# Kernel tuning notes

Measured on AMD Instinct MI355X. Metric: run time of the kernel, lower is better.

Reference implementation:

```python
import jax, jax.numpy as jnp
import numpy as np

B, N, D = 4, 2048, 512
H, DA, DL = 8, 64, 64  # heads, attention_dim, linear_dim
EPS = 1e-6


def _layer_norm(x, eps=EPS):
    # F.layer_norm with no affine params
    mu = jnp.mean(x, axis=-1, keepdims=True)
    var = jnp.var(x, axis=-1, keepdims=True)
    return (x - mu) * jax.lax.rsqrt(var + eps)


def setup_inputs() -> dict:
    key = jax.random.key(0)
    k1, k2, k3, k4 = jax.random.split(key, 4)
    x = jax.random.normal(k1, (B, N, D), dtype=jnp.float32)
    # causal (lower-triangular) valid-attention mask, float {0,1}, shape (B,1,N,N)
    attention_mask = jnp.broadcast_to(
        jnp.tril(jnp.ones((N, N), dtype=jnp.float32))[None, None], (B, 1, N, N)
    )
    # _uvqk: (D, 2*H*DL + 2*H*DA), init normal(0, 0.02)
    uvqk = 0.02 * jax.random.normal(k2, (D, 2 * H * DL + 2 * H * DA), dtype=jnp.float32)
    # _o: Linear(H*DL -> D), xavier uniform
    fan_in, fan_out = H * DL, D
    limit = float(np.sqrt(6.0 / (fan_in + fan_out)))
    o_weight = jax.random.uniform(k3, (fan_out, fan_in), dtype=jnp.float32, minval=-limit, maxval=limit)
    o_bias = jnp.zeros((D,), dtype=jnp.float32)
    return {"x": x, "attention_mask": attention_mask, "uvqk": uvqk,
            "o_weight": o_weight, "o_bias": o_bias}


def reference(x, attention_mask, uvqk, o_weight, o_bias):
    b, n, _ = x.shape
    normed_x = _layer_norm(x)
    mm = jax.nn.silu(normed_x @ uvqk)  # fused uvqk projection + silu
    u, v, q, k = jnp.split(mm, [H * DL, 2 * H * DL, 2 * H * DL + H * DA], axis=-1)
    qh = q.reshape(b, n, H, DA)
    kh = k.reshape(b, n, H, DA)
    vh = v.reshape(b, n, H, DL)
    # silu-activated (non-softmax) attention with mask
    qk = jnp.einsum('bnhd,bmhd->bhnm', qh, kh)
    qk = jax.nn.silu(qk) / n
    qk = qk * attention_mask  # (B,1,N,N) broadcast over heads
    attn = jnp.einsum('bhnm,bmhd->bnhd', qk, vh).reshape(b, n, H * DL)
    # gated norm + output proj + residual
    o_input = u * _layer_norm(attn)
    return o_input @ o_weight.T + o_bias + x
```

## Files before the change

### kernel.cpp

```cpp
#include <hip/hip_runtime.h>

typedef __bf16 bf16x8 __attribute__((ext_vector_type(8)));
typedef float f32x4 __attribute__((ext_vector_type(4)));
typedef float f32x16 __attribute__((ext_vector_type(16)));
typedef int i32x2 __attribute__((ext_vector_type(2)));

__device__ __forceinline__ unsigned short f2bf(float f) {
  return __builtin_bit_cast(unsigned short, (__bf16)f);
}
__device__ __forceinline__ float bfu2f(unsigned short b) {
  unsigned int u = ((unsigned int)b) << 16;
  return __builtin_bit_cast(float, u);
}
__device__ __forceinline__ float silu_f(float x) {
  return x * __builtin_amdgcn_rcpf(1.0f + __expf(-x));
}
__device__ __forceinline__ unsigned pk2(float a, float b) {
  return (unsigned)f2bf(a) | ((unsigned)f2bf(b) << 16);
}

template<int CPR, int NI, int SWZ>
__device__ __forceinline__ void stage16(const __bf16* __restrict__ g, int ld,
                                        __bf16* lds, int wave, int lane) {
#pragma unroll
  for (int t = 0; t < NI; ++t) {
    int cb = (wave * NI + t) * 64;
    int c = cb + lane;
    int row = c / CPR;
    int colb = (c % CPR) ^ (row & SWZ);
    __builtin_amdgcn_global_load_lds(
        (const __attribute__((address_space(1))) unsigned int*)(g + row * ld + colb * 8),
        (__attribute__((address_space(3))) unsigned int*)(lds + cb * 8),
        16, 0, 0);
  }
}

__global__ void k_prep(const float* __restrict__ x, __bf16* __restrict__ nx,
                       const float* __restrict__ ow, __bf16* __restrict__ owb,
                       const float* __restrict__ uvqk, __bf16* __restrict__ uvqkT) {
  int bid = blockIdx.x, tid = threadIdx.x;
  if (bid < 4096) {
    int t = tid & 127;
    int r = bid * 2 + (tid >> 7);
    int wave = tid >> 6;
    float4 v = ((const float4*)(x + (size_t)r * 512))[t];
    float s = v.x + v.y + v.z + v.w;
    float ss = v.x * v.x + v.y * v.y + v.z * v.z + v.w * v.w;
#pragma unroll
    for (int o = 32; o > 0; o >>= 1) { s += __shfl_down(s, o); ss += __shfl_down(ss, o); }
    __shared__ float red[4][2];
    if ((tid & 63) == 0) { red[wave][0] = s; red[wave][1] = ss; }
    __syncthreads();
    int rw = (wave >> 1) * 2;
    s = red[rw][0] + red[rw + 1][0];
    ss = red[rw][1] + red[rw + 1][1];
    float mu = s * (1.0f / 512.0f);
    float var = ss * (1.0f / 512.0f) - mu * mu;
    float rs = rsqrtf(var + 1e-6f);
    ushort4 o4;
    o4.x = f2bf((v.x - mu) * rs); o4.y = f2bf((v.y - mu) * rs);
    o4.z = f2bf((v.z - mu) * rs); o4.w = f2bf((v.w - mu) * rs);
    ((ushort4*)(nx + (size_t)r * 512))[t] = o4;
  } else if (bid < 4352) {
    int i = (bid - 4096) * 256 + tid;
    float4 v = ((const float4*)ow)[i];
    ushort4 o4;
    o4.x = f2bf(v.x); o4.y = f2bf(v.y); o4.z = f2bf(v.z); o4.w = f2bf(v.w);
    ((ushort4*)owb)[i] = o4;
  } else {
    __shared__ float tile[32][33];
    int bb = bid - 4352;
    int n0 = (bb & 63) * 32, k0 = (bb >> 6) * 32;
    int tx = tid & 31, ty = tid >> 5;
    for (int i = ty; i < 32; i += 8)
      tile[i][tx] = uvqk[(k0 + i) * 2048 + n0 + tx];
    __syncthreads();
    for (int i = ty; i < 32; i += 8)
      uvqkT[(n0 + i) * 512 + k0 + tx] = (__bf16)tile[tx][i];
  }
}

__global__ __launch_bounds__(256, 2) void k_proj(
    const __bf16* __restrict__ A, const __bf16* __restrict__ Bt,
    __bf16* __restrict__ u, __bf16* __restrict__ qn,
    __bf16* __restrict__ kn, __bf16* __restrict__ vt) {
  __shared__ __bf16 As[128 * 64];
  __shared__ __bf16 Bs[256 * 64];
  int tid = threadIdx.x, wave = tid >> 6, lane = tid & 63;
  int lr = lane & 15, lq = lane >> 4;
  int bn = blockIdx.x, bm = blockIdx.y;
  const __bf16* Ag = A + (size_t)bm * 128 * 512;
  const __bf16* Bg = Bt + (size_t)bn * 256 * 512;
  int wm = (wave >> 1) * 64, wn2 = (wave & 1) * 128;
  f32x4 acc[4][8] = {};
  for (int k0 = 0; k0 < 512; k0 += 64) {
    stage16<8, 4, 7>(Ag + k0, 512, As, wave, lane);
    stage16<8, 8, 7>(Bg + k0, 512, Bs, wave, lane);
    __syncthreads();
#pragma unroll
    for (int kk = 0; kk < 2; ++kk) {
      int b = kk * 4 + lq;
      bf16x8 a[4], bb[8];
#pragma unroll
      for (int i = 0; i < 4; ++i) {
        int row = wm + i * 16 + lr;
        a[i] = *(const bf16x8*)(As + row * 64 + ((b ^ (row & 7)) * 8));
      }
#pragma unroll
      for (int j = 0; j < 8; ++j) {
        int row = wn2 + j * 16 + lr;
        bb[j] = *(const bf16x8*)(Bs + row * 64 + ((b ^ (row & 7)) * 8));
      }
#pragma unroll
      for (int i = 0; i < 4; ++i)
#pragma unroll
        for (int j = 0; j < 8; ++j)
          acc[i][j] = __builtin_amdgcn_mfma_f32_16x16x32_bf16(a[i], bb[j], acc[i][j], 0, 0, 0);
    }
    __syncthreads();
  }
  int seg = bn >> 1;
  int cb = (bn & 1) * 256 + wn2;
  int rb0 = bm * 128 + wm + lq * 4;
  if (seg == 1) {
#pragma unroll
    for (int i = 0; i < 4; ++i) {
      int rb = rb0 + i * 16;
      int b = rb >> 11, n = rb & 2047;
#pragma unroll
      for (int j = 0; j < 8; ++j) {
        int c = cb + j * 16 + lr;
        ushort4 w;
        w.x = f2bf(silu_f(acc[i][j][0]) * (1.0f / 2048.0f));
        w.y = f2bf(silu_f(acc[i][j][1]) * (1.0f / 2048.0f));
        w.z = f2bf(silu_f(acc[i][j][2]) * (1.0f / 2048.0f));
        w.w = f2bf(silu_f(acc[i][j][3]) * (1.0f / 2048.0f));
        *(ushort4*)(vt + ((size_t)(b * 512 + c)) * 2048 + n) = w;
      }
    }
  } else {
    __bf16* dst = (seg == 0) ? u : ((seg == 2) ? qn : kn);
#pragma unroll
    for (int i = 0; i < 4; ++i) {
      int rb = rb0 + i * 16;
#pragma unroll
      for (int j = 0; j < 8; ++j) {
        int c = cb + j * 16 + lr;
#pragma unroll
        for (int rg = 0; rg < 4; ++rg)
          dst[(size_t)(rb + rg) * 512 + c] = (__bf16)silu_f(acc[i][j][rg]);
      }
    }
  }
}

__device__ __forceinline__ void attn_finish(
    const f32x16& s, int m0, int n0, int l31, int lh, int ms, bool natural,
    const __bf16* Vc, f32x16 po[2]) {
  bool dt = (m0 + 31 > n0);
  unsigned pk[8];
#pragma unroll
  for (int q = 0; q < 8; ++q) {
    float p01[2];
#pragma unroll
    for (int h = 0; h < 2; ++h) {
      int r = 2 * q + h;
      float xx = s[r];
      float pv = xx * __builtin_amdgcn_rcpf(1.0f + __expf(-xx));
      if (dt) {
        int mrow = m0 + 4 * lh + (r & 3) + 8 * (r >> 2);
        if (mrow > n0 + l31) pv = 0.0f;
      }
      p01[h] = pv;
    }
    pk[q] = pk2(p01[0], p01[1]);
  }
  i32x2 r0 = __builtin_amdgcn_permlane32_swap((int)pk[0], (int)pk[2], false, false);
  i32x2 r1 = __builtin_amdgcn_permlane32_swap((int)pk[1], (int)pk[3], false, false);
  i32x2 r2 = __builtin_amdgcn_permlane32_swap((int)pk[4], (int)pk[6], false, false);
  i32x2 r3 = __builtin_amdgcn_permlane32_swap((int)pk[5], (int)pk[7], false, false);
  union { bf16x8 v; unsigned u[4]; } f0, f1;
  if (natural) {
    f0.u[0] = r0.x; f0.u[2] = r0.y; f0.u[1] = r1.x; f0.u[3] = r1.y;
    f1.u[0] = r2.x; f1.u[2] = r2.y; f1.u[1] = r3.x; f1.u[3] = r3.y;
  } else {
    f0.u[0] = r0.y; f0.u[2] = r0.x; f0.u[1] = r1.y; f0.u[3] = r1.x;
    f1.u[0] = r2.y; f1.u[2] = r2.x; f1.u[1] = r3.y; f1.u[3] = r3.x;
  }
  bf16x8 pf[2] = { f0.v, f1.v };
#pragma unroll
  for (int t2 = 0; t2 < 2; ++t2) {
#pragma unroll
    for (int idl = 0; idl < 2; ++idl) {
      int row = idl * 32 + l31;
      bf16x8 av = *(const bf16x8*)(Vc + row * 64 +
          (((ms * 4 + t2 * 2 + lh) ^ (row & 7)) * 8));
      po[idl] = __builtin_amdgcn_mfma_f32_32x32x16_bf16(av, pf[t2], po[idl], 0, 0, 0);
    }
  }
}

__global__ __launch_bounds__(256, 4) void k_attn(
    const __bf16* __restrict__ qn, const __bf16* __restrict__ kn,
    const __bf16* __restrict__ vt, __bf16* __restrict__ oa,
    __bf16* __restrict__ ob, __bf16* __restrict__ oc,
    __bf16* __restrict__ od, int nz) {
  __shared__ __bf16 lds[16384];
  __bf16* Kb0 = lds;
  __bf16* Kb1 = lds + 4096;
  __bf16* Vb0 = lds + 8192;
  __bf16* Vb1 = lds + 12288;
  __bf16* bo = lds;

  int bh = blockIdx.x, p = blockIdx.y, z = blockIdx.z;
  int b = bh >> 3, hd = bh & 7;
  int tid = threadIdx.x, wave = tid >> 6, lane = tid & 63;
  int l31 = lane & 31, lh = lane >> 5;
  int wsl = (wave + p + z + bh) & 3;
  const __bf16* Kg = kn + (size_t)(b * 2048) * 512 + hd * 64;
  const __bf16* Vg = vt + (size_t)(b * 512 + hd * 64) * 2048;
  __bf16* Oz = (z == 0) ? oa : ((z == 1) ? ob : ((z == 2) ? oc : od));

  i32x2 pr = __builtin_amdgcn_permlane32_swap(lh ? 10 : 11, lh ? 20 : 21, false, false);
  bool natural = (__builtin_amdgcn_readfirstlane(pr.x) == 11);

  for (int ph = 0; ph < 2; ++ph) {
    int t = ph ? (15 - p) : p;
    int T = 2 * t + 2;
    int mlo = z * T / nz;
    int cnt = (z + 1) * T / nz - mlo;
    int n0 = t * 128 + wsl * 32;
    if (ph) __syncthreads();
    const __bf16* Qg = qn + (size_t)(b * 2048 + n0 + l31) * 512 + hd * 64 + lh * 8;
    bf16x8 qf[4];
#pragma unroll
    for (int ks = 0; ks < 4; ++ks) qf[ks] = *(const bf16x8*)(Qg + ks * 16);
    if (cnt > 0) {
      stage16<8, 2, 7>(Kg + (size_t)mlo * 64 * 512, 512, Kb0, wave, lane);
      stage16<8, 2, 7>(Vg + mlo * 64, 2048, Vb0, wave, lane);
    }
    __syncthreads();

    f32x16 po[2] = {};

    for (int i = 0; i < cnt; ++i) {
      int mt = mlo + i;
      const __bf16* Kc = (i & 1) ? Kb1 : Kb0;
      const __bf16* Vc = (i & 1) ? Vb1 : Vb0;
      if (i + 1 < cnt) {
        __bf16* Kn_ = (i & 1) ? Kb0 : Kb1;
        __bf16* Vn_ = (i & 1) ? Vb0 : Vb1;
        stage16<8, 2, 7>(Kg + (size_t)(mt + 1) * 64 * 512, 512, Kn_, wave, lane);
        stage16<8, 2, 7>(Vg + (mt + 1) * 64, 2048, Vn_, wave, lane);
      }
      int m0a = mt * 64, m0b = mt * 64 + 32;
      bool a0 = (m0a <= n0 + 31);
      bool a1 = (m0b <= n0 + 31);
      f32x16 s0 = {}, s1 = {};
      if (a0) {
#pragma unroll
        for (int ks = 0; ks < 4; ++ks) {
          int row = l31;
          bf16x8 ak = *(const bf16x8*)(Kc + row * 64 + (((ks * 2 + lh) ^ (row & 7)) * 8));
          s0 = __builtin_amdgcn_mfma_f32_32x32x16_bf16(ak, qf[ks], s0, 0, 0, 0);
        }
      }
      if (a1) {
#pragma unroll
        for (int ks = 0; ks < 4; ++ks) {
          int row = 32 + l31;
          bf16x8 ak = *(const bf16x8*)(Kc + row * 64 + (((ks * 2 + lh) ^ (row & 7)) * 8));
          s1 = __builtin_amdgcn_mfma_f32_32x32x16_bf16(ak, qf[ks], s1, 0, 0, 0);
        }
      }
      if (a0) attn_finish(s0, m0a, n0, l31, lh, 0, natural, Vc, po);
      if (a1) attn_finish(s1, m0b, n0, l31, lh, 1, natural, Vc, po);
      __syncthreads();
    }

    {
      int nrow = wsl * 32 + l31;
#pragma unroll
      for (int idl = 0; idl < 2; ++idl) {
#pragma unroll
        for (int g = 0; g < 4; ++g) {
          int dl0 = idl * 32 + g * 8 + lh * 4;
          int addr = nrow * 64 + ((((dl0 >> 3) ^ (nrow & 7)) << 3) | (dl0 & 7));
          ushort4 w;
          w.x = f2bf(po[idl][4 * g + 0]); w.y = f2bf(po[idl][4 * g + 1]);
          w.z = f2bf(po[idl][4 * g + 2]); w.w = f2bf(po[idl][4 * g + 3]);
          *(ushort4*)(bo + addr) = w;
        }
      }
    }
    __syncthreads();
    {
      int n = tid >> 1, cc = (tid & 1) * 32;
      __bf16* gdst = Oz + (size_t)(b * 2048 + t * 128 + n) * 512 + hd * 64 + cc;
#pragma unroll
      for (int kk2 = 0; kk2 < 4; ++kk2) {
        int dlb = cc + kk2 * 8;
        int a = n * 64 + (((dlb >> 3) ^ (n & 7)) << 3);
        *(uint4*)(gdst + kk2 * 8) = *(const uint4*)(bo + a);
      }
    }
  }
}

__global__ void k_oinput(const __bf16* __restrict__ oa, const __bf16* __restrict__ ob,
                         const __bf16* __restrict__ oc, const __bf16* __restrict__ od,
                         const __bf16* __restrict__ u, __bf16* __restrict__ oin,
                         int nz) {
  int r = blockIdx.x, t = threadIdx.x;
  ushort4 a4 = ((const ushort4*)(oa + (size_t)r * 512))[t];
  ushort4 b4 = ((const ushort4*)(ob + (size_t)r * 512))[t];
  ushort4 c4 = ((const ushort4*)(oc + (size_t)r * 512))[t];
  float e0 = 0.f, e1 = 0.f, e2 = 0.f, e3 = 0.f;
  if (nz == 4) {
    ushort4 d4 = ((const ushort4*)(od + (size_t)r * 512))[t];
    e0 = bfu2f(d4.x); e1 = bfu2f(d4.y); e2 = bfu2f(d4.z); e3 = bfu2f(d4.w);
  }
  float a0 = bfu2f(a4.x) + bfu2f(b4.x) + bfu2f(c4.x) + e0;
  float a1 = bfu2f(a4.y) + bfu2f(b4.y) + bfu2f(c4.y) + e1;
  float a2 = bfu2f(a4.z) + bfu2f(b4.z) + bfu2f(c4.z) + e2;
  float a3 = bfu2f(a4.w) + bfu2f(b4.w) + bfu2f(c4.w) + e3;
  float s = a0 + a1 + a2 + a3;
  float ss = a0 * a0 + a1 * a1 + a2 * a2 + a3 * a3;
#pragma unroll
  for (int o = 32; o > 0; o >>= 1) { s += __shfl_down(s, o); ss += __shfl_down(ss, o); }
  __shared__ float red[4];
  if ((t & 63) == 0) { red[(t >> 6) * 2] = s; red[(t >> 6) * 2 + 1] = ss; }
  __syncthreads();
  s = red[0] + red[2]; ss = red[1] + red[3];
  float mu = s * (1.0f / 512.0f);
  float var = ss * (1.0f / 512.0f) - mu * mu;
  float rs = rsqrtf(var + 1e-6f);
  ushort4 u4 = ((const ushort4*)(u + (size_t)r * 512))[t];
  ushort4 o4;
  o4.x = f2bf(bfu2f(u4.x) * (a0 - mu) * rs);
  o4.y = f2bf(bfu2f(u4.y) * (a1 - mu) * rs);
  o4.z = f2bf(bfu2f(u4.z) * (a2 - mu) * rs);
  o4.w = f2bf(bfu2f(u4.w) * (a3 - mu) * rs);
  ((ushort4*)(oin + (size_t)r * 512))[t] = o4;
}

__global__ __launch_bounds__(256, 4) void k_out(
    const __bf16* __restrict__ A, const __bf16* __restrict__ Bt,
    const float* __restrict__ bias, const float* __restrict__ x,
    float* __restrict__ out) {
  __shared__ __bf16 As[64 * 64];
  __shared__ __bf16 Bs[128 * 64];
  int tid = threadIdx.x, wave = tid >> 6, lane = tid & 63;
  int lr = lane & 15, lq = lane >> 4;
  int bn = blockIdx.x, bm = blockIdx.y;
  const __bf16* Ag = A + (size_t)bm * 64 * 512;
  const __bf16* Bg = Bt + (size_t)bn * 128 * 512;
  int wm = (wave >> 1) * 32, wn = (wave & 1) * 64;
  f32x4 acc[2][4] = {};
  for (int k0 = 0; k0 < 512; k0 += 64) {
    stage16<8, 2, 7>(Ag + k0, 512, As, wave, lane);
    stage16<8, 4, 7>(Bg + k0, 512, Bs, wave, lane);
    __syncthreads();
#pragma unroll
    for (int kk = 0; kk < 2; ++kk) {
      int b = kk * 4 + lq;
      bf16x8 a[2], bb[4];
#pragma unroll
      for (int i = 0; i < 2; ++i) {
        int row = wm + i * 16 + lr;
        a[i] = *(const bf16x8*)(As + row * 64 + ((b ^ (row & 7)) * 8));
      }
#pragma unroll
      for (int j = 0; j < 4; ++j) {
        int row = wn + j * 16 + lr;
        bb[j] = *(const bf16x8*)(Bs + row * 64 + ((b ^ (row & 7)) * 8));
      }
#pragma unroll
      for (int i = 0; i < 2; ++i)
#pragma unroll
        for (int j = 0; j < 4; ++j)
          acc[i][j] = __builtin_amdgcn_mfma_f32_16x16x32_bf16(a[i], bb[j], acc[i][j], 0, 0, 0);
    }
    __syncthreads();
  }
  int cb = bn * 128 + wn;
  int rb0 = bm * 64 + wm + lq * 4;
#pragma unroll
  for (int j = 0; j < 4; ++j) {
    int c = cb + j * 16 + lr;
    float bv = bias[c];
#pragma unroll
    for (int i = 0; i < 2; ++i) {
      int rb = rb0 + i * 16;
#pragma unroll
      for (int rg = 0; rg < 4; ++rg) {
        size_t idx = (size_t)(rb + rg) * 512 + c;
        out[idx] = acc[i][j][rg] + bv + x[idx];
      }
    }
  }
}

extern "C" void kernel_launch(void* const* d_in, const int* in_sizes, int n_in,
                              void* d_out, int out_size, void* d_ws, size_t ws_size,
                              hipStream_t stream) {
  const float* x = (const float*)d_in[0];
  const float* uvqk = (const float*)d_in[2];
  const float* ow = (const float*)d_in[3];
  const float* obias = (const float*)d_in[4];
  float* out = (float*)d_out;

  char* w = (char*)d_ws;
  const size_t MB8 = 8u * 1024 * 1024;
  __bf16* nx    = (__bf16*)(w);
  __bf16* u     = (__bf16*)(w + MB8);
  __bf16* qn    = (__bf16*)(w + 2 * MB8);
  __bf16* kn    = (__bf16*)(w + 3 * MB8);
  __bf16* vt    = (__bf16*)(w + 4 * MB8);
  __bf16* uvqkT = (__bf16*)(w + 5 * MB8);
  __bf16* owb   = (__bf16*)(w + 5 * MB8 + 2097152);
  size_t od_off = 5 * MB8 + 2097152 + 524288;
  __bf16* Oa    = nx;
  __bf16* Ob    = (__bf16*)d_out;
  __bf16* Oc    = (__bf16*)d_out + (size_t)8192 * 512;
  __bf16* Od    = (__bf16*)(w + od_off);
  __bf16* o_in  = qn;

  int nz = (ws_size >= od_off + MB8) ? 4 : 3;

  k_prep<<<5376, 256, 0, stream>>>(x, nx, ow, owb, uvqk, uvqkT);
  k_proj<<<dim3(8, 64), 256, 0, stream>>>(nx, uvqkT, u, qn, kn, vt);
  k_attn<<<dim3(32, 8, nz), 256, 0, stream>>>(qn, kn, vt, Oa, Ob, Oc, Od, nz);
  k_oinput<<<8192, 128, 0, stream>>>(Oa, Ob, Oc, Od, u, o_in, nz);
  k_out<<<dim3(4, 128), 256, 0, stream>>>(o_in, owb, obias, x, out);
}
```

Measured before the change: 200.5 us.

## Triple-buffer K/V staging with explicit waitcnt, add MFMA priority, fix split at three

The attention kernel moves from double to triple buffering of K/V tiles in LDS. It issues two tiles ahead and replaces the per-iteration __syncthreads with an explicit vmcnt wait plus a barrier, so only one barrier per tile is needed. MFMA sections are wrapped in s_setprio to favour matrix issue across waves. The key-split factor is hard-coded to 3, dropping the optional fourth partial buffer, and launch bounds drop to 3 blocks per CU because LDS use grows. This risks lower occupancy and less parallelism where four splits were previously available, and relies on the hand-counted vmcnt value matching the loads stage16 issues.

```diff
diff --git a/kernel.cpp b/kernel.cpp
--- a/kernel.cpp
+++ b/kernel.cpp
@@ -188,6 +188,7 @@
     f1.u[0] = r2.y; f1.u[2] = r2.x; f1.u[1] = r3.y; f1.u[3] = r3.x;
   }
   bf16x8 pf[2] = { f0.v, f1.v };
+  __builtin_amdgcn_s_setprio(1);
 #pragma unroll
   for (int t2 = 0; t2 < 2; ++t2) {
 #pragma unroll
@@ -198,18 +199,14 @@
       po[idl] = __builtin_amdgcn_mfma_f32_32x32x16_bf16(av, pf[t2], po[idl], 0, 0, 0);
     }
   }
-}
-
-__global__ __launch_bounds__(256, 4) void k_attn(
+  __builtin_amdgcn_s_setprio(0);
+}
+
+__global__ __launch_bounds__(256, 3) void k_attn(
     const __bf16* __restrict__ qn, const __bf16* __restrict__ kn,
     const __bf16* __restrict__ vt, __bf16* __restrict__ oa,
-    __bf16* __restrict__ ob, __bf16* __restrict__ oc,
-    __bf16* __restrict__ od, int nz) {
-  __shared__ __bf16 lds[16384];
-  __bf16* Kb0 = lds;
-  __bf16* Kb1 = lds + 4096;
-  __bf16* Vb0 = lds + 8192;
-  __bf16* Vb1 = lds + 12288;
+    __bf16* __restrict__ ob, __bf16* __restrict__ oc) {
+  __shared__ __bf16 lds[24576];
   __bf16* bo = lds;
 
   int bh = blockIdx.x, p = blockIdx.y, z = blockIdx.z;
@@ -219,7 +216,7 @@
   int wsl = (wave + p + z + bh) & 3;
   const __bf16* Kg = kn + (size_t)(b * 2048) * 512 + hd * 64;
   const __bf16* Vg = vt + (size_t)(b * 512 + hd * 64) * 2048;
-  __bf16* Oz = (z == 0) ? oa : ((z == 1) ? ob : ((z == 2) ? oc : od));
+  __bf16* Oz = (z == 0) ? oa : ((z == 1) ? ob : oc);
 
   i32x2 pr = __builtin_amdgcn_permlane32_swap(lh ? 10 : 11, lh ? 20 : 21, false, false);
   bool natural = (__builtin_amdgcn_readfirstlane(pr.x) == 11);
@@ -227,8 +224,8 @@
   for (int ph = 0; ph < 2; ++ph) {
     int t = ph ? (15 - p) : p;
     int T = 2 * t + 2;
-    int mlo = z * T / nz;
-    int cnt = (z + 1) * T / nz - mlo;
+    int mlo = z * T / 3;
+    int cnt = (z + 1) * T / 3 - mlo;
     int n0 = t * 128 + wsl * 32;
     if (ph) __syncthreads();
     const __bf16* Qg = qn + (size_t)(b * 2048 + n0 + l31) * 512 + hd * 64 + lh * 8;
@@ -236,47 +233,63 @@
 #pragma unroll
     for (int ks = 0; ks < 4; ++ks) qf[ks] = *(const bf16x8*)(Qg + ks * 16);
     if (cnt > 0) {
-      stage16<8, 2, 7>(Kg + (size_t)mlo * 64 * 512, 512, Kb0, wave, lane);
-      stage16<8, 2, 7>(Vg + mlo * 64, 2048, Vb0, wave, lane);
-    }
-    __syncthreads();
+      stage16<8, 2, 7>(Kg + (size_t)mlo * 64 * 512, 512, lds, wave, lane);
+      stage16<8, 2, 7>(Vg + mlo * 64, 2048, lds + 12288, wave, lane);
+    }
+    if (cnt > 1) {
+      stage16<8, 2, 7>(Kg + (size_t)(mlo + 1) * 64 * 512, 512, lds + 4096, wave, lane);
+      stage16<8, 2, 7>(Vg + (mlo + 1) * 64, 2048, lds + 16384, wave, lane);
+    }
 
     f32x16 po[2] = {};
+    int cur = 0;
 
     for (int i = 0; i < cnt; ++i) {
+      if (i + 1 < cnt) {
+        asm volatile("s_waitcnt vmcnt(4)" ::: "memory");
+      } else {
+        asm volatile("s_waitcnt vmcnt(0)" ::: "memory");
+      }
+      __builtin_amdgcn_sched_barrier(0);
+      __builtin_amdgcn_s_barrier();
+      __builtin_amdgcn_sched_barrier(0);
+      if (i + 2 < cnt) {
+        int bs = (cur == 0) ? 2 : cur - 1;
+        stage16<8, 2, 7>(Kg + (size_t)(mlo + i + 2) * 64 * 512, 512, lds + bs * 4096, wave, lane);
+        stage16<8, 2, 7>(Vg + (mlo + i + 2) * 64, 2048, lds + 12288 + bs * 4096, wave, lane);
+      }
+      const __bf16* Kc = lds + cur * 4096;
+      const __bf16* Vc = lds + 12288 + cur * 4096;
       int mt = mlo + i;
-      const __bf16* Kc = (i & 1) ? Kb1 : Kb0;
-      const __bf16* Vc = (i & 1) ? Vb1 : Vb0;
-      if (i + 1 < cnt) {
-        __bf16* Kn_ = (i & 1) ? Kb0 : Kb1;
-        __bf16* Vn_ = (i & 1) ? Vb0 : Vb1;
-        stage16<8, 2, 7>(Kg + (size_t)(mt + 1) * 64 * 512, 512, Kn_, wave, lane);
-        stage16<8, 2, 7>(Vg + (mt + 1) * 64, 2048, Vn_, wave, lane);
-      }
       int m0a = mt * 64, m0b = mt * 64 + 32;
       bool a0 = (m0a <= n0 + 31);
       bool a1 = (m0b <= n0 + 31);
       f32x16 s0 = {}, s1 = {};
       if (a0) {
+        __builtin_amdgcn_s_setprio(1);
 #pragma unroll
         for (int ks = 0; ks < 4; ++ks) {
           int row = l31;
           bf16x8 ak = *(const bf16x8*)(Kc + row * 64 + (((ks * 2 + lh) ^ (row & 7)) * 8));
           s0 = __builtin_amdgcn_mfma_f32_32x32x16_bf16(ak, qf[ks], s0, 0, 0, 0);
         }
+        __builtin_amdgcn_s_setprio(0);
       }
       if (a1) {
+        __builtin_amdgcn_s_setprio(1);
 #pragma unroll
         for (int ks = 0; ks < 4; ++ks) {
           int row = 32 + l31;
           bf16x8 ak = *(const bf16x8*)(Kc + row * 64 + (((ks * 2 + lh) ^ (row & 7)) * 8));
           s1 = __builtin_amdgcn_mfma_f32_32x32x16_bf16(ak, qf[ks], s1, 0, 0, 0);
         }
+        __builtin_amdgcn_s_setprio(0);
       }
       if (a0) attn_finish(s0, m0a, n0, l31, lh, 0, natural, Vc, po);
       if (a1) attn_finish(s1, m0b, n0, l31, lh, 1, natural, Vc, po);
-      __syncthreads();
-    }
+      cur = (cur == 2) ? 0 : cur + 1;
+    }
+    __syncthreads();
 
     {
       int nrow = wsl * 32 + l31;
@@ -308,22 +321,16 @@
 }
 
 __global__ void k_oinput(const __bf16* __restrict__ oa, const __bf16* __restrict__ ob,
-                         const __bf16* __restrict__ oc, const __bf16* __restrict__ od,
-                         const __bf16* __restrict__ u, __bf16* __restrict__ oin,
-                         int nz) {
+                         const __bf16* __restrict__ oc, const __bf16* __restrict__ u,
+                         __bf16* __restrict__ oin) {
   int r = blockIdx.x, t = threadIdx.x;
   ushort4 a4 = ((const ushort4*)(oa + (size_t)r * 512))[t];
   ushort4 b4 = ((const ushort4*)(ob + (size_t)r * 512))[t];
   ushort4 c4 = ((const ushort4*)(oc + (size_t)r * 512))[t];
-  float e0 = 0.f, e1 = 0.f, e2 = 0.f, e3 = 0.f;
-  if (nz == 4) {
-    ushort4 d4 = ((const ushort4*)(od + (size_t)r * 512))[t];
-    e0 = bfu2f(d4.x); e1 = bfu2f(d4.y); e2 = bfu2f(d4.z); e3 = bfu2f(d4.w);
-  }
-  float a0 = bfu2f(a4.x) + bfu2f(b4.x) + bfu2f(c4.x) + e0;
-  float a1 = bfu2f(a4.y) + bfu2f(b4.y) + bfu2f(c4.y) + e1;
-  float a2 = bfu2f(a4.z) + bfu2f(b4.z) + bfu2f(c4.z) + e2;
-  float a3 = bfu2f(a4.w) + bfu2f(b4.w) + bfu2f(c4.w) + e3;
+  float a0 = bfu2f(a4.x) + bfu2f(b4.x) + bfu2f(c4.x);
+  float a1 = bfu2f(a4.y) + bfu2f(b4.y) + bfu2f(c4.y);
+  float a2 = bfu2f(a4.z) + bfu2f(b4.z) + bfu2f(c4.z);
+  float a3 = bfu2f(a4.w) + bfu2f(b4.w) + bfu2f(c4.w);
   float s = a0 + a1 + a2 + a3;
   float ss = a0 * a0 + a1 * a1 + a2 * a2 + a3 * a3;
 #pragma unroll
@@ -419,18 +426,14 @@
   __bf16* vt    = (__bf16*)(w + 4 * MB8);
   __bf16* uvqkT = (__bf16*)(w + 5 * MB8);
   __bf16* owb   = (__bf16*)(w + 5 * MB8 + 2097152);
-  size_t od_off = 5 * MB8 + 2097152 + 524288;
   __bf16* Oa    = nx;
   __bf16* Ob    = (__bf16*)d_out;
   __bf16* Oc    = (__bf16*)d_out + (size_t)8192 * 512;
-  __bf16* Od    = (__bf16*)(w + od_off);
   __bf16* o_in  = qn;
-
-  int nz = (ws_size >= od_off + MB8) ? 4 : 3;
 
   k_prep<<<5376, 256, 0, stream>>>(x, nx, ow, owb, uvqk, uvqkT);
   k_proj<<<dim3(8, 64), 256, 0, stream>>>(nx, uvqkT, u, qn, kn, vt);
-  k_attn<<<dim3(32, 8, nz), 256, 0, stream>>>(qn, kn, vt, Oa, Ob, Oc, Od, nz);
-  k_oinput<<<8192, 128, 0, stream>>>(Oa, Ob, Oc, Od, u, o_in, nz);
+  k_attn<<<dim3(32, 8, 3), 256, 0, stream>>>(qn, kn, vt, Oa, Ob, Oc);
+  k_oinput<<<8192, 128, 0, stream>>>(Oa, Ob, Oc, u, o_in);
   k_out<<<dim3(4, 128), 256, 0, stream>>>(o_in, owb, obias, x, out);
 }
```

Measured after the change: 198.0 us. About the same (-1.3%).

## Read K/V directly from global memory per wave, drop LDS staging and barriers

Applied to the files above, without the earlier changes.

The attention kernel no longer stages K and V tiles into double-buffered LDS behind per-tile __syncthreads. Each wave now reads its K rows and V^T columns straight from global memory (relying on the cache) and walks its own 32-wide key subtiles independently. Full subtiles and the diagonal subtile are split with a template flag so the causal mask test only runs on the diagonal. s_setprio hints are wrapped around the MFMA sections. This removes barrier stalls and LDS traffic at the cost of uncoalesced global/L2 loads per wave, and it also drops the per-block wave-slice rotation.

```diff
diff --git a/kernel.cpp b/kernel.cpp
--- a/kernel.cpp
+++ b/kernel.cpp
@@ -154,10 +154,20 @@
   }
 }
 
-__device__ __forceinline__ void attn_finish(
-    const f32x16& s, int m0, int n0, int l31, int lh, int ms, bool natural,
-    const __bf16* Vc, f32x16 po[2]) {
-  bool dt = (m0 + 31 > n0);
+template<bool DT>
+__device__ __forceinline__ void attn_subtile(
+    int m0, int n0, int l31, int lh, bool natural,
+    const __bf16* __restrict__ Kg, const __bf16* __restrict__ Vg,
+    const bf16x8 qf[4], f32x16 po[2]) {
+  const __bf16* kp = Kg + (size_t)(m0 + l31) * 512 + lh * 8;
+  f32x16 s = {};
+  __builtin_amdgcn_s_setprio(1);
+#pragma unroll
+  for (int ks = 0; ks < 4; ++ks) {
+    bf16x8 ak = *(const bf16x8*)(kp + ks * 16);
+    s = __builtin_amdgcn_mfma_f32_32x32x16_bf16(ak, qf[ks], s, 0, 0, 0);
+  }
+  __builtin_amdgcn_s_setprio(0);
   unsigned pk[8];
 #pragma unroll
   for (int q = 0; q < 8; ++q) {
@@ -167,7 +177,7 @@
       int r = 2 * q + h;
       float xx = s[r];
       float pv = xx * __builtin_amdgcn_rcpf(1.0f + __expf(-xx));
-      if (dt) {
+      if (DT) {
         int mrow = m0 + 4 * lh + (r & 3) + 8 * (r >> 2);
         if (mrow > n0 + l31) pv = 0.0f;
       }
@@ -188,16 +198,17 @@
     f1.u[0] = r2.y; f1.u[2] = r2.x; f1.u[1] = r3.y; f1.u[3] = r3.x;
   }
   bf16x8 pf[2] = { f0.v, f1.v };
+  const __bf16* vp = Vg + (size_t)l31 * 2048 + m0 + lh * 8;
+  __builtin_amdgcn_s_setprio(1);
 #pragma unroll
   for (int t2 = 0; t2 < 2; ++t2) {
 #pragma unroll
     for (int idl = 0; idl < 2; ++idl) {
-      int row = idl * 32 + l31;
-      bf16x8 av = *(const bf16x8*)(Vc + row * 64 +
-          (((ms * 4 + t2 * 2 + lh) ^ (row & 7)) * 8));
+      bf16x8 av = *(const bf16x8*)(vp + (size_t)idl * 32 * 2048 + t2 * 16);
       po[idl] = __builtin_amdgcn_mfma_f32_32x32x16_bf16(av, pf[t2], po[idl], 0, 0, 0);
     }
   }
+  __builtin_amdgcn_s_setprio(0);
 }
 
 __global__ __launch_bounds__(256, 4) void k_attn(
@@ -205,18 +216,12 @@
     const __bf16* __restrict__ vt, __bf16* __restrict__ oa,
     __bf16* __restrict__ ob, __bf16* __restrict__ oc,
     __bf16* __restrict__ od, int nz) {
-  __shared__ __bf16 lds[16384];
-  __bf16* Kb0 = lds;
-  __bf16* Kb1 = lds + 4096;
-  __bf16* Vb0 = lds + 8192;
-  __bf16* Vb1 = lds + 12288;
-  __bf16* bo = lds;
+  __shared__ __bf16 bo[128 * 64];
 
   int bh = blockIdx.x, p = blockIdx.y, z = blockIdx.z;
   int b = bh >> 3, hd = bh & 7;
   int tid = threadIdx.x, wave = tid >> 6, lane = tid & 63;
   int l31 = lane & 31, lh = lane >> 5;
-  int wsl = (wave + p + z + bh) & 3;
   const __bf16* Kg = kn + (size_t)(b * 2048) * 512 + hd * 64;
   const __bf16* Vg = vt + (size_t)(b * 512 + hd * 64) * 2048;
   __bf16* Oz = (z == 0) ? oa : ((z == 1) ? ob : ((z == 2) ? oc : od));
@@ -227,59 +232,25 @@
   for (int ph = 0; ph < 2; ++ph) {
     int t = ph ? (15 - p) : p;
     int T = 2 * t + 2;
-    int mlo = z * T / nz;
-    int cnt = (z + 1) * T / nz - mlo;
-    int n0 = t * 128 + wsl * 32;
+    int u_lo = 2 * (z * T / nz);
+    int u_hi_z = 2 * ((z + 1) * T / nz);
+    int n0 = t * 128 + wave * 32;
     if (ph) __syncthreads();
     const __bf16* Qg = qn + (size_t)(b * 2048 + n0 + l31) * 512 + hd * 64 + lh * 8;
     bf16x8 qf[4];
 #pragma unroll
     for (int ks = 0; ks < 4; ++ks) qf[ks] = *(const bf16x8*)(Qg + ks * 16);
-    if (cnt > 0) {
-      stage16<8, 2, 7>(Kg + (size_t)mlo * 64 * 512, 512, Kb0, wave, lane);
-      stage16<8, 2, 7>(Vg + mlo * 64, 2048, Vb0, wave, lane);
-    }
-    __syncthreads();
 
     f32x16 po[2] = {};
-
-    for (int i = 0; i < cnt; ++i) {
-      int mt = mlo + i;
-      const __bf16* Kc = (i & 1) ? Kb1 : Kb0;
-      const __bf16* Vc = (i & 1) ? Vb1 : Vb0;
-      if (i + 1 < cnt) {
-        __bf16* Kn_ = (i & 1) ? Kb0 : Kb1;
-        __bf16* Vn_ = (i & 1) ? Vb0 : Vb1;
-        stage16<8, 2, 7>(Kg + (size_t)(mt + 1) * 64 * 512, 512, Kn_, wave, lane);
-        stage16<8, 2, 7>(Vg + (mt + 1) * 64, 2048, Vn_, wave, lane);
-      }
-      int m0a = mt * 64, m0b = mt * 64 + 32;
-      bool a0 = (m0a <= n0 + 31);
-      bool a1 = (m0b <= n0 + 31);
-      f32x16 s0 = {}, s1 = {};
-      if (a0) {
-#pragma unroll
-        for (int ks = 0; ks < 4; ++ks) {
-          int row = l31;
-          bf16x8 ak = *(const bf16x8*)(Kc + row * 64 + (((ks * 2 + lh) ^ (row & 7)) * 8));
-          s0 = __builtin_amdgcn_mfma_f32_32x32x16_bf16(ak, qf[ks], s0, 0, 0, 0);
-        }
-      }
-      if (a1) {
-#pragma unroll
-        for (int ks = 0; ks < 4; ++ks) {
-          int row = 32 + l31;
-          bf16x8 ak = *(const bf16x8*)(Kc + row * 64 + (((ks * 2 + lh) ^ (row & 7)) * 8));
-          s1 = __builtin_amdgcn_mfma_f32_32x32x16_bf16(ak, qf[ks], s1, 0, 0, 0);
-        }
-      }
-      if (a0) attn_finish(s0, m0a, n0, l31, lh, 0, natural, Vc, po);
-      if (a1) attn_finish(s1, m0b, n0, l31, lh, 1, natural, Vc, po);
-      __syncthreads();
-    }
+    int u_d = n0 >> 5;
+    int u_hi_full = min(u_hi_z, u_d);
+    for (int u = u_lo; u < u_hi_full; ++u)
+      attn_subtile<false>(u * 32, n0, l31, lh, natural, Kg, Vg, qf, po);
+    if (u_d >= u_lo && u_d < u_hi_z)
+      attn_subtile<true>(n0, n0, l31, lh, natural, Kg, Vg, qf, po);
 
     {
-      int nrow = wsl * 32 + l31;
+      int nrow = wave * 32 + l31;
 #pragma unroll
       for (int idl = 0; idl < 2; ++idl) {
 #pragma unroll
```

New measurement: 229.4 us. +14.4%, slower.
